# Kernel tuning notes

Measured on AMD Instinct MI355X. Metric: run time of the kernel, lower is better.

## Reference

```python
import jax, jax.numpy as jnp
import numpy as np

FEAT = 256
HID = FEAT // 2
N_KEYS = 2          # output_keys = ["energy_0", "energy_1"]
N_MOLS = 2000
ATOMS_PER_MOL = 100
N_ATOMS = N_MOLS * ATOMS_PER_MOL
LOG2 = 0.6931471805599453


def shifted_softplus(x):
    # NFF's shifted softplus: softplus(x) - log(2)
    return jax.nn.softplus(x) - LOG2


def setup_inputs() -> dict:
    key = jax.random.key(0)
    ks = jax.random.split(key, 6)
    s_i = jax.random.normal(ks[0], (N_ATOMS, FEAT), dtype=jnp.float32)
    xyz = jax.random.normal(ks[1], (N_ATOMS, 3), dtype=jnp.float32)
    num_atoms = jnp.full((N_MOLS,), ATOMS_PER_MOL, dtype=jnp.int64)
    # Per-key MLP params stacked over keys: Linear(F->H), act, Linear(H->1)
    W1 = jax.random.normal(ks[2], (N_KEYS, FEAT, HID), dtype=jnp.float32) / np.sqrt(FEAT)
    b1 = jnp.zeros((N_KEYS, HID), dtype=jnp.float32)
    W2 = jax.random.normal(ks[3], (N_KEYS, HID), dtype=jnp.float32) / np.sqrt(HID)
    b2 = jnp.zeros((N_KEYS,), dtype=jnp.float32)
    return {"s_i": s_i, "xyz": xyz, "num_atoms": num_atoms,
            "W1": W1, "b1": b1, "W2": W2, "b2": b2}


def reference(s_i, xyz, num_atoms, W1, b1, W2, b2):
    n_mols = num_atoms.shape[0]
    # segment id per atom, replacing the torch.split(...)+per-chunk sum loop
    seg = jnp.repeat(jnp.arange(n_mols), num_atoms,
                     total_repeat_length=s_i.shape[0])        # [N]
    # per-key MLP: [K,N,H] hidden, [K,N] scalar output per atom
    h = shifted_softplus(jnp.einsum('nf,kfh->knh', s_i, W1) + b1[:, None, :])
    val = jnp.einsum('knh,kh->kn', h, W2) + b2[:, None]       # [K, N]
    # fused segment-sum pooling -> per-molecule scalars
    pooled = jax.ops.segment_sum(val.T, seg, num_segments=n_mols)  # [M, K]
    return pooled.T                                            # [K, M]
```

## Files before the change

### kernel.cpp

```cpp
#include <hip/hip_runtime.h>

#define FEAT 256
#define HID 128
#define NKEYS 2

typedef __bf16 bf16x8 __attribute__((ext_vector_type(8)));
typedef float f32x16 __attribute__((ext_vector_type(16)));

union Frag {
    bf16x8 v;
    unsigned u[4];
    uint4 q;
};

__device__ __forceinline__ unsigned pack_bf16_2(float f0, float f1) {
    unsigned u0 = __float_as_uint(f0) + 0x8000u;
    unsigned u1 = __float_as_uint(f1) + 0x8000u;
    return __builtin_amdgcn_perm(u1, u0, 0x07060302u);
}

__device__ __forceinline__ float ssp(float x) {
    float sp = __logf(1.0f + __expf(x));
    sp = (x > 15.0f) ? x : sp;
    return sp - 0.69314718056f;
}

__device__ __forceinline__ int find_mol(const int* off, int n_mols, int g) {
    int lo = 0, hi = n_mols;
    while (hi - lo > 1) {
        int mid = (lo + hi) >> 1;
        if (off[mid] <= g) lo = mid; else hi = mid;
    }
    return lo;
}

__device__ __forceinline__ void gload_lds16(const float* g, void* l) {
    __builtin_amdgcn_global_load_lds(
        (const __attribute__((address_space(1))) unsigned int*)g,
        (__attribute__((address_space(3))) unsigned int*)l,
        16, 0, 0);
}

__global__ void prep_kernel(const void* __restrict__ num_atoms_raw,
                            const float* __restrict__ W1,
                            int n_mols, int n_atoms,
                            int* __restrict__ off,
                            unsigned short* __restrict__ Bp,
                            float* __restrict__ out, int out_n) {
    if (blockIdx.x > 0) {
        int idx = (blockIdx.x - 1) * 256 + threadIdx.x;
        int c = idx >> 8;
        int k = idx & 255;
        int key = c >> 7, j = c & 127;
        float f = W1[(size_t)key * FEAT * HID + (size_t)k * HID + j];
        unsigned u = __float_as_uint(f);
        unsigned r = (u + 0x7FFFu + ((u >> 16) & 1u)) >> 16;
        Bp[(size_t)c * FEAT + k] = (unsigned short)r;
        return;
    }
    for (int i = threadIdx.x; i < out_n; i += 256) out[i] = 0.0f;

    __shared__ long long tsum[256];
    __shared__ int csum[256];
    int tid = threadIdx.x;
    const int* a32 = (const int*)num_atoms_raw;
    const long long* a64 = (const long long*)num_atoms_raw;
    int chunk = (n_mols + 255) >> 8;
    int lo = tid * chunk;
    if (lo > n_mols) lo = n_mols;
    int hi = lo + chunk;
    if (hi > n_mols) hi = n_mols;

    long long s32 = 0;
    for (int i = lo; i < hi; ++i) s32 += (long long)a32[i];
    tsum[tid] = s32;
    __syncthreads();
    #pragma unroll
    for (int d = 128; d > 0; d >>= 1) {
        if (tid < d) tsum[tid] += tsum[tid + d];
        __syncthreads();
    }
    int mode = (tsum[0] == (long long)n_atoms) ? 0 : 1;
    long long s = s32;
    if (mode) {
        s = 0;
        for (int i = lo; i < hi; ++i) s += a64[i];
    }
    int v = (int)s;
    csum[tid] = v;
    __syncthreads();
    #pragma unroll
    for (int d = 1; d < 256; d <<= 1) {
        int t = (tid >= d) ? csum[tid - d] : 0;
        __syncthreads();
        csum[tid] += t;
        __syncthreads();
    }
    int run = csum[tid] - v;
    for (int i = lo; i < hi; ++i) {
        off[i] = run;
        run += mode ? (int)a64[i] : a32[i];
    }
    if (hi >= n_mols) off[n_mols] = run;
}

__global__ __launch_bounds__(512, 4)
void gemm_fused(const float* __restrict__ A,
                const unsigned short* __restrict__ Bp,
                const float* __restrict__ b1,
                const float* __restrict__ W2,
                const float* __restrict__ b2,
                const int* __restrict__ off,
                float* __restrict__ out,
                int n_atoms, int n_mols, int ntiles, int stride) {
    __shared__ uint4  ldsA[2][1024];
    __shared__ int    offlds[2048];
    __shared__ float  part[8][64];
    __shared__ int    rowmol[64];
    __shared__ float  molacc[NKEYS][4];

    const int tid  = threadIdx.x;
    const int lane = tid & 63;
    const int wid  = tid >> 6;
    const int l31  = lane & 31;
    const int half = lane >> 5;

    const bool lds_ok = (n_mols + 1) <= 2048;
    if (lds_ok) ((int4*)offlds)[tid] = ((const int4*)off)[tid];
    if (tid < NKEYS * 4) molacc[tid >> 2][tid & 3] = 0.0f;

    const int c0 = wid * 32 + l31;
    const unsigned short* bb = Bp + (size_t)c0 * FEAT + half * 8;
    const float b1c  = b1[c0];
    const float w2c  = W2[c0];
    const float b2k0 = b2[0], b2k1 = b2[1];
    const int rB = l31 + 32;
    const int x  = l31 & 15;

    auto stage = [&](int tile, int c, int buf) {
        const int m0s = tile * 64;
        #pragma unroll
        for (int i = 0; i < 2; ++i) {
            const int pos = wid * 128 + i * 64;
            const int r   = (pos >> 4) + (lane >> 4);
            const int u   = (lane & 15) ^ (r & 15);
            int gr = m0s + r;
            if (gr > n_atoms - 1) gr = n_atoms - 1;
            gload_lds16(A + (size_t)gr * FEAT + c * 64 + u * 4,
                        (void*)(&ldsA[buf][pos]));
        }
    };

    int t = blockIdx.x;
    int cur = 0;
    stage(t, 0, 0);
    __syncthreads();

    for (; t < ntiles; t += stride) {
        const int m0 = t * 64;
        f32x16 acc0 = 0.0f, acc1 = 0.0f;

        #pragma unroll
        for (int c = 0; c < 4; ++c) {
            Frag bw[4];
            #pragma unroll
            for (int j = 0; j < 4; ++j)
                bw[j].q = *(const uint4*)(bb + c * 64 + j * 16);
            __builtin_amdgcn_sched_barrier(0);

            const bool last = (c == 3) && (t + stride >= ntiles);
            if (!last) stage((c < 3) ? t : (t + stride), (c + 1) & 3, cur ^ 1);

            if (c == 0 && (tid & 7) == 0) {
                int r = tid >> 3;
                int gm = m0 + r;
                if (gm > n_atoms - 1) gm = n_atoms - 1;
                rowmol[r] = lds_ok ? find_mol(offlds, n_mols, gm)
                                   : find_mol(off, n_mols, gm);
            }

            const uint4* lbuf = ldsA[cur];
            #pragma unroll
            for (int ks = 0; ks < 4; ++ks) {
                const int us = (ks * 4 + half * 2) ^ x;
                uint4 lo0 = lbuf[l31 * 16 + us];
                uint4 hi0 = lbuf[l31 * 16 + (us ^ 1)];
                uint4 lo1 = lbuf[rB  * 16 + us];
                uint4 hi1 = lbuf[rB  * 16 + (us ^ 1)];
                const float4 fl0 = *(const float4*)&lo0;
                const float4 fh0 = *(const float4*)&hi0;
                const float4 fl1 = *(const float4*)&lo1;
                const float4 fh1 = *(const float4*)&hi1;
                Frag a0, a1;
                a0.u[0] = pack_bf16_2(fl0.x, fl0.y);
                a0.u[1] = pack_bf16_2(fl0.z, fl0.w);
                a0.u[2] = pack_bf16_2(fh0.x, fh0.y);
                a0.u[3] = pack_bf16_2(fh0.z, fh0.w);
                a1.u[0] = pack_bf16_2(fl1.x, fl1.y);
                a1.u[1] = pack_bf16_2(fl1.z, fl1.w);
                a1.u[2] = pack_bf16_2(fh1.x, fh1.y);
                a1.u[3] = pack_bf16_2(fh1.z, fh1.w);
                acc0 = __builtin_amdgcn_mfma_f32_32x32x16_bf16(a0.v, bw[ks].v, acc0, 0, 0, 0);
                acc1 = __builtin_amdgcn_mfma_f32_32x32x16_bf16(a1.v, bw[ks].v, acc1, 0, 0, 0);
            }

            __syncthreads();
            cur ^= 1;
        }

        #pragma unroll
        for (int rt = 0; rt < 2; ++rt) {
            const f32x16& Ac = rt ? acc1 : acc0;
            #pragma unroll
            for (int r = 0; r < 16; ++r) {
                float v = ssp(Ac[r] + b1c) * w2c;
                v += __shfl_xor(v, 1);
                v += __shfl_xor(v, 2);
                v += __shfl_xor(v, 4);
                v += __shfl_xor(v, 8);
                v += __shfl_xor(v, 16);
                if (l31 == r) {
                    int row = rt * 32 + (r & 3) + 8 * (r >> 2) + 4 * half;
                    part[wid][row] = v;
                }
            }
        }
        __syncthreads();

        if (tid < NKEYS * 64) {
            int k = tid >> 6, r = tid & 63;
            int gm = m0 + r;
            if (gm < n_atoms) {
                float val = part[4 * k][r] + part[4 * k + 1][r]
                          + part[4 * k + 2][r] + part[4 * k + 3][r]
                          + (k ? b2k1 : b2k0);
                int mol = rowmol[r];
                int ml  = mol - rowmol[0];
                if (ml < 4) atomicAdd(&molacc[k][ml], val);
                else        atomicAdd(&out[(size_t)k * n_mols + mol], val);
            }
        }
        __syncthreads();

        if (tid < NKEYS * 4) {
            int k = tid >> 2, ml = tid & 3;
            int mol = rowmol[0] + ml;
            if (mol < n_mols) {
                float v = molacc[k][ml];
                if (v != 0.0f) atomicAdd(&out[(size_t)k * n_mols + mol], v);
                molacc[k][ml] = 0.0f;
            }
        }
    }
}

extern "C" void kernel_launch(void* const* d_in, const int* in_sizes, int n_in,
                              void* d_out, int out_size, void* d_ws, size_t ws_size,
                              hipStream_t stream) {
    const float* s_i      = (const float*)d_in[0];
    const void*  num_atoms = d_in[2];
    const float* W1 = (const float*)d_in[3];
    const float* b1 = (const float*)d_in[4];
    const float* W2 = (const float*)d_in[5];
    const float* b2 = (const float*)d_in[6];
    int n_atoms = in_sizes[0] / FEAT;
    int n_mols  = in_sizes[2];
    float* out = (float*)d_out;

    int* off = (int*)d_ws;
    size_t off_bytes = (((size_t)(n_mols + 1) * 4) + 255) & ~(size_t)255;
    if (off_bytes < 8192) off_bytes = 8192;
    unsigned short* Bp = (unsigned short*)((char*)d_ws + off_bytes);

    int pack_blocks = (NKEYS * HID * FEAT) / 256;
    prep_kernel<<<1 + pack_blocks, 256, 0, stream>>>(num_atoms, W1, n_mols, n_atoms,
                                                     off, Bp, out, out_size);

    int ntiles  = (n_atoms + 63) / 64;
    int nblocks = ntiles < 512 ? ntiles : 512;
    gemm_fused<<<nblocks, 512, 0, stream>>>(s_i, Bp, b1, W2, b2, off, out,
                                            n_atoms, n_mols, ntiles, nblocks);
}
```

Before: 375.5 us.

## Triple-buffer A tiles with prefetch distance two and lighter barriers

The shared-memory A staging grows from two buffers to three, so global-to-LDS loads are issued two k-chunks ahead instead of one. The single end-of-chunk __syncthreads is replaced by a raw s_barrier at the start of each chunk, with an LDS-count wait only on the first chunk and in the epilogue. The aim is to hide global load latency behind the MFMA work and cut barrier overhead. The cost is about 16 KB more LDS per block, which may reduce the number of resident blocks. Correctness depends on the compiler still inserting a vmcnt wait before the LDS reads of the DMA-filled buffers.

```diff
diff --git a/kernel.cpp b/kernel.cpp
--- a/kernel.cpp
+++ b/kernel.cpp
@@ -39,6 +39,18 @@
         (const __attribute__((address_space(1))) unsigned int*)g,
         (__attribute__((address_space(3))) unsigned int*)l,
         16, 0, 0);
+}
+
+__device__ __forceinline__ void bar_raw() {
+    __builtin_amdgcn_sched_barrier(0);
+    __builtin_amdgcn_s_barrier();
+    __builtin_amdgcn_sched_barrier(0);
+}
+__device__ __forceinline__ void bar_lds() {
+    __builtin_amdgcn_sched_barrier(0);
+    asm volatile("s_waitcnt lgkmcnt(0)" ::: "memory");
+    __builtin_amdgcn_s_barrier();
+    __builtin_amdgcn_sched_barrier(0);
 }
 
 __global__ void prep_kernel(const void* __restrict__ num_atoms_raw,
@@ -113,7 +125,7 @@
                 const int* __restrict__ off,
                 float* __restrict__ out,
                 int n_atoms, int n_mols, int ntiles, int stride) {
-    __shared__ uint4  ldsA[2][1024];
+    __shared__ uint4  ldsA[3][1024];
     __shared__ int    offlds[2048];
     __shared__ float  part[8][64];
     __shared__ int    rowmol[64];
@@ -137,7 +149,7 @@
     const int rB = l31 + 32;
     const int x  = l31 & 15;
 
-    auto stage = [&](int tile, int c, int buf) {
+    auto stage = [&](int tile, int cc, int buf) {
         const int m0s = tile * 64;
         #pragma unroll
         for (int i = 0; i < 2; ++i) {
@@ -146,30 +158,39 @@
             const int u   = (lane & 15) ^ (r & 15);
             int gr = m0s + r;
             if (gr > n_atoms - 1) gr = n_atoms - 1;
-            gload_lds16(A + (size_t)gr * FEAT + c * 64 + u * 4,
+            gload_lds16(A + (size_t)gr * FEAT + cc * 64 + u * 4,
                         (void*)(&ldsA[buf][pos]));
         }
     };
 
     int t = blockIdx.x;
+    stage(t, 0, 0);
+    stage(t, 1, 1);
+    __syncthreads();
+
     int cur = 0;
-    stage(t, 0, 0);
-    __syncthreads();
-
     for (; t < ntiles; t += stride) {
         const int m0 = t * 64;
         f32x16 acc0 = 0.0f, acc1 = 0.0f;
 
         #pragma unroll
         for (int c = 0; c < 4; ++c) {
+            if (c == 0) bar_lds(); else bar_raw();
+
             Frag bw[4];
             #pragma unroll
             for (int j = 0; j < 4; ++j)
                 bw[j].q = *(const uint4*)(bb + c * 64 + j * 16);
             __builtin_amdgcn_sched_barrier(0);
 
-            const bool last = (c == 3) && (t + stride >= ntiles);
-            if (!last) stage((c < 3) ? t : (t + stride), (c + 1) & 3, cur ^ 1);
+            {
+                const int t2 = (c < 2) ? t : (t + stride);
+                if (t2 < ntiles) {
+                    int nb = cur + 2; if (nb >= 3) nb -= 3;
+                    stage(t2, (c + 2) & 3, nb);
+                }
+            }
+            __builtin_amdgcn_sched_barrier(0);
 
             if (c == 0 && (tid & 7) == 0) {
                 int r = tid >> 3;
@@ -179,33 +200,36 @@
                                    : find_mol(off, n_mols, gm);
             }
 
-            const uint4* lbuf = ldsA[cur];
+            const uint4* lbuf = &ldsA[cur][0];
             #pragma unroll
             for (int ks = 0; ks < 4; ++ks) {
                 const int us = (ks * 4 + half * 2) ^ x;
-                uint4 lo0 = lbuf[l31 * 16 + us];
-                uint4 hi0 = lbuf[l31 * 16 + (us ^ 1)];
-                uint4 lo1 = lbuf[rB  * 16 + us];
-                uint4 hi1 = lbuf[rB  * 16 + (us ^ 1)];
-                const float4 fl0 = *(const float4*)&lo0;
-                const float4 fh0 = *(const float4*)&hi0;
-                const float4 fl1 = *(const float4*)&lo1;
-                const float4 fh1 = *(const float4*)&hi1;
-                Frag a0, a1;
-                a0.u[0] = pack_bf16_2(fl0.x, fl0.y);
-                a0.u[1] = pack_bf16_2(fl0.z, fl0.w);
-                a0.u[2] = pack_bf16_2(fh0.x, fh0.y);
-                a0.u[3] = pack_bf16_2(fh0.z, fh0.w);
-                a1.u[0] = pack_bf16_2(fl1.x, fl1.y);
-                a1.u[1] = pack_bf16_2(fl1.z, fl1.w);
-                a1.u[2] = pack_bf16_2(fh1.x, fh1.y);
-                a1.u[3] = pack_bf16_2(fh1.z, fh1.w);
-                acc0 = __builtin_amdgcn_mfma_f32_32x32x16_bf16(a0.v, bw[ks].v, acc0, 0, 0, 0);
-                acc1 = __builtin_amdgcn_mfma_f32_32x32x16_bf16(a1.v, bw[ks].v, acc1, 0, 0, 0);
-            }
-
-            __syncthreads();
-            cur ^= 1;
+                {
+                    uint4 lo = lbuf[l31 * 16 + us];
+                    uint4 hi = lbuf[l31 * 16 + (us ^ 1)];
+                    const float4 fl = *(const float4*)&lo;
+                    const float4 fh = *(const float4*)&hi;
+                    Frag a0;
+                    a0.u[0] = pack_bf16_2(fl.x, fl.y);
+                    a0.u[1] = pack_bf16_2(fl.z, fl.w);
+                    a0.u[2] = pack_bf16_2(fh.x, fh.y);
+                    a0.u[3] = pack_bf16_2(fh.z, fh.w);
+                    acc0 = __builtin_amdgcn_mfma_f32_32x32x16_bf16(a0.v, bw[ks].v, acc0, 0, 0, 0);
+                }
+                {
+                    uint4 lo = lbuf[rB * 16 + us];
+                    uint4 hi = lbuf[rB * 16 + (us ^ 1)];
+                    const float4 fl = *(const float4*)&lo;
+                    const float4 fh = *(const float4*)&hi;
+                    Frag a1;
+                    a1.u[0] = pack_bf16_2(fl.x, fl.y);
+                    a1.u[1] = pack_bf16_2(fl.z, fl.w);
+                    a1.u[2] = pack_bf16_2(fh.x, fh.y);
+                    a1.u[3] = pack_bf16_2(fh.z, fh.w);
+                    acc1 = __builtin_amdgcn_mfma_f32_32x32x16_bf16(a1.v, bw[ks].v, acc1, 0, 0, 0);
+                }
+            }
+            cur = (cur >= 2) ? 0 : cur + 1;
         }
 
         #pragma unroll
@@ -225,7 +249,7 @@
                 }
             }
         }
-        __syncthreads();
+        bar_lds();
 
         if (tid < NKEYS * 64) {
             int k = tid >> 6, r = tid & 63;
@@ -240,7 +264,7 @@
                 else        atomicAdd(&out[(size_t)k * n_mols + mol], val);
             }
         }
-        __syncthreads();
+        bar_lds();
 
         if (tid < NKEYS * 4) {
             int k = tid >> 2, ml = tid & 3;
```

New measurement: 349.1 us. 1.08x faster.
